# Kernel tuning notes

Hardware: AMD Instinct MI355X
Metric: run time of the kernel (lower is better)

Reference implementation:

```python
import jax, jax.numpy as jnp
import numpy as np
import math

B, T, H, NH, L = 8, 256, 128, 2, 2
DH = H // NH
KC = 3
ITEMNUM = 50000
TIME_SPAN = 256
PERIODS = jnp.array([86400.0, 604800.0, 2592000.0], dtype=jnp.float32)
SCALE_MAGS = [1.0, 1.0, 1.0]
NEG = -1e9


def layernorm(x, g, b, eps=1e-8):
    mu = x.mean(-1, keepdims=True)
    var = ((x - mu) ** 2).mean(-1, keepdims=True)
    return (x - mu) / jnp.sqrt(var + eps) * g + b


def time_encode(t, time_proj):
    # HarmonicTimeEncoding: [sin(2*pi*t/c), cos(2*pi*t/c)] per cycle -> Linear(2K->H, no bias)
    phase = 2.0 * math.pi * t[..., None] / PERIODS
    enc = jnp.concatenate([jnp.sin(phase), jnp.cos(phase)], axis=-1)  # (..., 2K)
    return enc @ time_proj.T


def phase_bias_fn(t, lambdas):
    # PhaseSimilarityBias: per-cycle cosine similarity of (sin,cos) phase vectors
    phase = 2.0 * math.pi * t[..., None] / PERIODS  # (B,T,K)
    phi = jnp.stack([jnp.sin(phase), jnp.cos(phase)], axis=-1)  # (B,T,K,2)
    phi = phi / jnp.maximum(jnp.linalg.norm(phi, axis=-1, keepdims=True), 1e-12)
    sim = jnp.einsum('btkd,bskd->btsk', phi, phi)
    return (sim * lambdas).sum(-1)  # (B,T,T)


def setup_inputs() -> dict:
    key = jax.random.key(0)
    ks = jax.random.split(key, 40)
    def n(i, shape, std=0.02):
        return jax.random.normal(ks[i], shape, dtype=jnp.float32) * std
    inp = {}
    inp['log_seqs'] = jax.random.randint(ks[0], (B, T), 0, ITEMNUM + 1)
    inp['time_matrices'] = jax.random.randint(ks[1], (B, T, T), 0, TIME_SPAN + 1)
    inp['time_seq'] = jnp.sort(jax.random.uniform(ks[2], (B, T), dtype=jnp.float32) * 5e6, axis=-1)
    inp['pos_seqs'] = jax.random.randint(ks[3], (B, T), 1, ITEMNUM + 1)
    inp['neg_seqs'] = jax.random.randint(ks[4], (B, T), 1, ITEMNUM + 1)
    inp['target_times'] = jax.random.uniform(ks[5], (B,), dtype=jnp.float32) * 5e6
    inp['item_emb'] = n(6, (ITEMNUM + 1, H)).at[0].set(0.0)  # padding_idx=0
    inp['abs_pos_K'] = n(7, (T, H))
    inp['abs_pos_V'] = n(8, (T, H))
    inp['time_K_emb'] = n(9, (TIME_SPAN + 1, H))
    inp['time_V_emb'] = n(10, (TIME_SPAN + 1, H))
    inp['Wq'] = n(11, (L, H, H), 0.05); inp['bq'] = jnp.zeros((L, H))
    inp['Wk'] = n(12, (L, H, H), 0.05); inp['bk'] = jnp.zeros((L, H))
    inp['Wv'] = n(13, (L, H, H), 0.05); inp['bv'] = jnp.zeros((L, H))
    inp['attn_ln_g'] = jnp.ones((L, H)); inp['attn_ln_b'] = jnp.zeros((L, H))
    inp['fwd_ln_g'] = jnp.ones((L, H)); inp['fwd_ln_b'] = jnp.zeros((L, H))
    inp['w1'] = n(14, (L, H, H), 0.05); inp['b1'] = jnp.zeros((L, H))
    inp['w2'] = n(15, (L, H, H), 0.05); inp['b2'] = jnp.zeros((L, H))
    inp['last_ln_g'] = jnp.ones((H,)); inp['last_ln_b'] = jnp.zeros((H,))
    inp['time_proj'] = n(16, (H, 2 * KC), 1.0 / math.sqrt(H))
    inp['lambdas'] = jnp.array(SCALE_MAGS, dtype=jnp.float32)
    inp['pred_W'] = n(17, (H, H), 0.05)
    inp['fus_W1'] = n(18, (H, 2 * H), 0.05); inp['fus_b1'] = jnp.zeros((H,))
    inp['fus_W2'] = n(19, (H, H), 0.05); inp['fus_b2'] = jnp.zeros((H,))
    return inp


def reference(log_seqs, time_matrices, time_seq, pos_seqs, neg_seqs, target_times,
              item_emb, abs_pos_K, abs_pos_V, time_K_emb, time_V_emb,
              Wq, bq, Wk, bk, Wv, bv, attn_ln_g, attn_ln_b, fwd_ln_g, fwd_ln_b,
              w1, b1, w2, b2, last_ln_g, last_ln_b, time_proj, lambdas,
              pred_W, fus_W1, fus_b1, fus_W2, fus_b2):
    seqs = item_emb[log_seqs] * math.sqrt(H)
    seqs = seqs + time_encode(time_seq, time_proj)
    tl_mask = (log_seqs == 0)  # (B,T) padding mask
    keep = (~tl_mask)[..., None].astype(seqs.dtype)
    seqs = seqs * keep
    absK = abs_pos_K.reshape(T, NH, DH).transpose(1, 0, 2)  # (NH,T,DH)
    absV = abs_pos_V.reshape(T, NH, DH).transpose(1, 0, 2)
    tK = time_K_emb[time_matrices].reshape(B, T, T, NH, DH)  # (B,T,T,NH,DH)
    tV = time_V_emb[time_matrices].reshape(B, T, T, NH, DH)
    pbias = phase_bias_fn(time_seq, lambdas)  # (B,T,T)
    causal = jnp.triu(jnp.ones((T, T), dtype=bool), k=1)
    mask = causal[None, None] | tl_mask[:, None, None, :]  # (B,1,T,T)
    for l in range(L):
        Qn = layernorm(seqs, attn_ln_g[l], attn_ln_b[l])
        q = (Qn @ Wq[l].T + bq[l]).reshape(B, T, NH, DH).transpose(0, 2, 1, 3)
        k = (seqs @ Wk[l].T + bk[l]).reshape(B, T, NH, DH).transpose(0, 2, 1, 3)
        v = (seqs @ Wv[l].T + bv[l]).reshape(B, T, NH, DH).transpose(0, 2, 1, 3)
        scores = jnp.einsum('bhqd,bhkd->bhqk', q, k)
        scores = scores + jnp.einsum('bhqd,hkd->bhqk', q, absK)
        scores = scores + jnp.einsum('bqkhd,bhqd->bhqk', tK, q)  # relative time-interval term
        scores = scores / math.sqrt(DH) + pbias[:, None]  # phase-similarity logit bias
        scores = jnp.where(mask, NEG, scores)
        A = jax.nn.softmax(scores, axis=-1)
        out = jnp.einsum('bhqk,bhkd->bhqd', A, v)
        out = out + jnp.einsum('bhqk,hkd->bhqd', A, absV)
        out = out + jnp.einsum('bhqk,bqkhd->bhqd', A, tV)
        out = out.transpose(0, 2, 1, 3).reshape(B, T, H)
        seqs = Qn + out
        x = layernorm(seqs, fwd_ln_g[l], fwd_ln_b[l])
        seqs = jax.nn.relu(x @ w1[l].T + b1[l]) @ w2[l].T + b2[l] + x
        seqs = seqs * keep
    log_feats = layernorm(seqs, last_ln_g, last_ln_b)
    H_per = time_encode(target_times, time_proj) @ pred_W.T  # (B,H)
    H_per = jnp.broadcast_to(H_per[:, None], (B, T, H))
    cat = jnp.concatenate([log_feats, H_per], axis=-1)
    fused = jax.nn.gelu(cat @ fus_W1.T + fus_b1, approximate=False) @ fus_W2.T + fus_b2
    pos_logits = (fused * item_emb[pos_seqs]).sum(-1)
    neg_logits = (fused * item_emb[neg_seqs]).sum(-1)
    return (pos_logits, neg_logits)
```

## Files before the change

kernel.cpp:

```cpp
#include <hip/hip_runtime.h>
#include <math.h>

#define TT 256
#define HH 128
#define QT 4

__device__ __forceinline__ void enc6(float t, float e[6]) {
  float x = 6.2831853071795864769f * t;
  float a0 = x / 86400.0f, a1 = x / 604800.0f, a2 = x / 2592000.0f;
  e[0] = sinf(a0); e[1] = sinf(a1); e[2] = sinf(a2);
  e[3] = cosf(a0); e[4] = cosf(a1); e[5] = cosf(a2);
}

__device__ __forceinline__ unsigned short f2bf(float x) {
  unsigned int u = __float_as_uint(x);
  u = (u + 0x7FFFu + ((u >> 16) & 1u)) >> 16;
  return (unsigned short)u;
}

__global__ __launch_bounds__(128) void embed_kernel(
    const int* __restrict__ log_seqs, const float* __restrict__ time_seq,
    const float* __restrict__ item_emb, const float* __restrict__ time_proj,
    float* __restrict__ seqs, float* __restrict__ sc6) {
  int row = blockIdx.x;
  int h = threadIdx.x;
  float t = time_seq[row];
  float e[6]; enc6(t, e);
  int idx = log_seqs[row];
  const float* tp = time_proj + h * 6;
  float val = item_emb[(size_t)idx * HH + h] * 11.313708498984761f;
  val += e[0]*tp[0] + e[1]*tp[1] + e[2]*tp[2] + e[3]*tp[3] + e[4]*tp[4] + e[5]*tp[5];
  seqs[(size_t)row * HH + h] = (idx != 0) ? val : 0.0f;
  if (h < 6) sc6[row * 6 + h] = e[h];
}

__global__ __launch_bounds__(128) void qkv_fused(
    const float* __restrict__ S,
    const float* __restrict__ Wq, const float* __restrict__ bq,
    const float* __restrict__ Wk, const float* __restrict__ bk,
    const float* __restrict__ Wv, const float* __restrict__ bv,
    const float* __restrict__ lng, const float* __restrict__ lnb,
    const float* __restrict__ absK, const float* __restrict__ absV,
    float* __restrict__ QN, float* __restrict__ QB,
    float* __restrict__ KB, float* __restrict__ VB) {
  int which = blockIdx.x >> 8;
  int m0 = (blockIdx.x & 255) * 8;
  int n = threadIdx.x;
  __shared__ float At[8][132];
  __shared__ float mu[8], rs[8];
  #pragma unroll
  for (int r = 0; r < 8; ++r) At[r][n] = S[(size_t)(m0 + r) * HH + n];
  __syncthreads();
  if (which == 0) {
    if (n < 64) {
      int r = n >> 3, sg = n & 7;
      float s = 0.f;
      #pragma unroll
      for (int i = 0; i < 16; ++i) s += At[r][sg * 16 + i];
      s += __shfl_xor(s, 1); s += __shfl_xor(s, 2); s += __shfl_xor(s, 4);
      if (sg == 0) mu[r] = s * (1.0f / HH);
    }
    __syncthreads();
    if (n < 64) {
      int r = n >> 3, sg = n & 7;
      float mm = mu[r], s = 0.f;
      #pragma unroll
      for (int i = 0; i < 16; ++i) { float d = At[r][sg*16+i] - mm; s += d * d; }
      s += __shfl_xor(s, 1); s += __shfl_xor(s, 2); s += __shfl_xor(s, 4);
      if (sg == 0) rs[r] = rsqrtf(s * (1.0f / HH) + 1e-8f);
    }
    __syncthreads();
    float gg = lng[n], bb = lnb[n];
    #pragma unroll
    for (int r = 0; r < 8; ++r) {
      float v = (At[r][n] - mu[r]) * rs[r] * gg + bb;
      At[r][n] = v;
      QN[(size_t)(m0 + r) * HH + n] = v;
    }
    __syncthreads();
  }
  const float* W    = which == 0 ? Wq : which == 1 ? Wk : Wv;
  const float* bias = which == 0 ? bq : which == 1 ? bk : bv;
  const float* addP = which == 1 ? absK : which == 2 ? absV : nullptr;
  float* dst        = which == 0 ? QB : which == 1 ? KB : VB;
  float acc[8];
  #pragma unroll
  for (int r = 0; r < 8; ++r) acc[r] = 0.f;
  const float* wr = W + (size_t)n * HH;
  for (int d = 0; d < HH; d += 4) {
    float4 w = *(const float4*)(wr + d);
    #pragma unroll
    for (int r = 0; r < 8; ++r) {
      float4 a = *(const float4*)(&At[r][d]);
      acc[r] = fmaf(a.x, w.x, fmaf(a.y, w.y, fmaf(a.z, w.z, fmaf(a.w, w.w, acc[r]))));
    }
  }
  float bn = bias[n];
  #pragma unroll
  for (int r = 0; r < 8; ++r) {
    int m = m0 + r;
    float v = acc[r] + bn;
    if (addP) v += addP[(size_t)(m & 255) * HH + n];
    dst[(size_t)m * HH + n] = v;
  }
}

__global__ __launch_bounds__(256) void attn_fused(
    const float* __restrict__ QB, const float* __restrict__ KB,
    const float* __restrict__ VB, const float* __restrict__ QN,
    const int* __restrict__ log_seqs, const int* __restrict__ tmat,
    const float* __restrict__ sc6, const float* __restrict__ tKe,
    const float* __restrict__ tVe, const float* __restrict__ lambdas,
    float* __restrict__ out) {
  int blk = blockIdx.x;
  int qt = blk & 63;
  int h = (blk >> 6) & 1;
  int b = blk >> 7;
  int q0 = qt << 2;
  int hoff = h << 6;
  int tid = threadIdx.x;

  __shared__ unsigned short tKs[257][64];
  __shared__ unsigned short tVs[257][64];
  __shared__ float Qt[QT][64];
  __shared__ float Pp[QT][256];
  __shared__ unsigned short tmq[QT][256];
  __shared__ float sk6[256 * 6];
  __shared__ float sq6[QT * 6];
  __shared__ unsigned char kmask[256];

  for (int idx = tid; idx < 257 * 16; idx += 256) {
    int row = idx >> 4, c4 = (idx & 15) << 2;
    float4 vk = *(const float4*)(tKe + (size_t)row * HH + hoff + c4);
    float4 vv = *(const float4*)(tVe + (size_t)row * HH + hoff + c4);
    uint2 a, c;
    a.x = (unsigned)f2bf(vk.x) | ((unsigned)f2bf(vk.y) << 16);
    a.y = (unsigned)f2bf(vk.z) | ((unsigned)f2bf(vk.w) << 16);
    c.x = (unsigned)f2bf(vv.x) | ((unsigned)f2bf(vv.y) << 16);
    c.y = (unsigned)f2bf(vv.z) | ((unsigned)f2bf(vv.w) << 16);
    *(uint2*)(&tKs[row][c4]) = a;
    *(uint2*)(&tVs[row][c4]) = c;
  }
  for (int idx = tid; idx < 256 * 6; idx += 256)
    sk6[idx] = sc6[(size_t)b * (256 * 6) + idx];
  { int q = tid >> 6, d = tid & 63;
    Qt[q][d] = QB[((size_t)(b * TT + q0 + q)) * HH + hoff + d]; }
  if (tid < QT * 6) sq6[tid] = sc6[((size_t)(b * TT + q0)) * 6 + tid];
  for (int idx = tid; idx < QT * 256; idx += 256) {
    int q = idx >> 8, k = idx & 255;
    tmq[q][k] = (unsigned short)tmat[((size_t)(b * TT + q0 + q)) * TT + k];
  }
  kmask[tid] = (log_seqs[b * TT + tid] == 0) ? 1 : 0;
  __syncthreads();

  int q = tid >> 6;
  int lane = tid & 63;
  int qg = q0 + q;
  float4 qreg[16];
  #pragma unroll
  for (int i = 0; i < 16; ++i) qreg[i] = *(const float4*)(&Qt[q][i << 2]);
  float l0 = lambdas[0], l1 = lambdas[1], l2 = lambdas[2];
  float sA = sq6[q*6+0], sB = sq6[q*6+1], sC = sq6[q*6+2];
  float cA = sq6[q*6+3], cB = sq6[q*6+4], cC = sq6[q*6+5];
  float sarr[4];
  #pragma unroll
  for (int j = 0; j < 4; ++j) {
    int k = lane + (j << 6);
    float sv = -1e9f;
    if (k <= qg && kmask[k] == 0) {
      int tm = tmq[q][k];
      const float* kp = KB + ((size_t)(b * TT + k)) * HH + hoff;
      float acc = 0.f;
      #pragma unroll
      for (int d4 = 0; d4 < 16; ++d4) {
        float4 kv = *(const float4*)(kp + (d4 << 2));
        uint2 tu = *(const uint2*)(&tKs[tm][d4 << 2]);
        float t0 = __uint_as_float(tu.x << 16);
        float t1 = __uint_as_float(tu.x & 0xFFFF0000u);
        float t2 = __uint_as_float(tu.y << 16);
        float t3 = __uint_as_float(tu.y & 0xFFFF0000u);
        float4 qv = qreg[d4];
        acc = fmaf(qv.x, kv.x + t0, acc);
        acc = fmaf(qv.y, kv.y + t1, acc);
        acc = fmaf(qv.z, kv.z + t2, acc);
        acc = fmaf(qv.w, kv.w + t3, acc);
      }
      const float* s6 = &sk6[k * 6];
      float pb = l0 * (sA * s6[0] + cA * s6[3])
               + l1 * (sB * s6[1] + cB * s6[4])
               + l2 * (sC * s6[2] + cC * s6[5]);
      sv = acc * 0.125f + pb;
    }
    sarr[j] = sv;
  }
  float m = fmaxf(fmaxf(sarr[0], sarr[1]), fmaxf(sarr[2], sarr[3]));
  #pragma unroll
  for (int o = 32; o > 0; o >>= 1) m = fmaxf(m, __shfl_xor(m, o));
  float p0 = __expf(sarr[0] - m), p1 = __expf(sarr[1] - m),
        p2 = __expf(sarr[2] - m), p3 = __expf(sarr[3] - m);
  float l = p0 + p1 + p2 + p3;
  #pragma unroll
  for (int o = 32; o > 0; o >>= 1) l += __shfl_xor(l, o);
  float inv = 1.0f / l;
  Pp[q][lane]       = p0 * inv;
  Pp[q][lane + 64]  = p1 * inv;
  Pp[q][lane + 128] = p2 * inv;
  Pp[q][lane + 192] = p3 * inv;
  __syncthreads();

  int kend = (m < -5e8f) ? 256 : (qg + 1);
  float oacc = 0.f;
  const float* vb = VB + ((size_t)(b * TT)) * HH + hoff + lane;
  #pragma unroll 4
  for (int k = 0; k < kend; ++k) {
    float pk = Pp[q][k];
    int tm = tmq[q][k];
    float v = vb[(size_t)k * HH];
    float tv = __uint_as_float(((unsigned)tVs[tm][lane]) << 16);
    oacc = fmaf(pk, v + tv, oacc);
  }
  size_t obase = ((size_t)(b * TT + qg)) * HH + hoff + lane;
  out[obase] = QN[obase] + oacc;
}

__global__ __launch_bounds__(128) void ffn_fused(
    const float* __restrict__ S, const float* __restrict__ W1, const float* __restrict__ b1,
    const float* __restrict__ W2, const float* __restrict__ b2,
    const float* __restrict__ lng, const float* __restrict__ lnb,
    const int* __restrict__ log_seqs, float* __restrict__ outS) {
  int m0 = blockIdx.x * 4;
  int n = threadIdx.x;
  __shared__ float Xt[4][132];
  __shared__ float Ht[4][132];
  __shared__ float mu[4], rs[4];
  #pragma unroll
  for (int r = 0; r < 4; ++r) Xt[r][n] = S[(size_t)(m0 + r) * HH + n];
  __syncthreads();
  if (n < 32) {
    int r = n >> 3, sg = n & 7;
    float s = 0.f;
    #pragma unroll
    for (int i = 0; i < 16; ++i) s += Xt[r][sg * 16 + i];
    s += __shfl_xor(s, 1); s += __shfl_xor(s, 2); s += __shfl_xor(s, 4);
    if (sg == 0) mu[r] = s * (1.0f / HH);
  }
  __syncthreads();
  if (n < 32) {
    int r = n >> 3, sg = n & 7;
    float mm = mu[r], s = 0.f;
    #pragma unroll
    for (int i = 0; i < 16; ++i) { float d = Xt[r][sg*16+i] - mm; s += d * d; }
    s += __shfl_xor(s, 1); s += __shfl_xor(s, 2); s += __shfl_xor(s, 4);
    if (sg == 0) rs[r] = rsqrtf(s * (1.0f / HH) + 1e-8f);
  }
  __syncthreads();
  float gg = lng[n], bb = lnb[n];
  #pragma unroll
  for (int r = 0; r < 4; ++r) Xt[r][n] = (Xt[r][n] - mu[r]) * rs[r] * gg + bb;
  __syncthreads();
  float acc[4] = {0.f, 0.f, 0.f, 0.f};
  const float* wr = W1 + (size_t)n * HH;
  for (int d = 0; d < HH; d += 4) {
    float4 w = *(const float4*)(wr + d);
    #pragma unroll
    for (int r = 0; r < 4; ++r) {
      float4 a = *(const float4*)(&Xt[r][d]);
      acc[r] = fmaf(a.x, w.x, fmaf(a.y, w.y, fmaf(a.z, w.z, fmaf(a.w, w.w, acc[r]))));
    }
  }
  float b1n = b1[n];
  #pragma unroll
  for (int r = 0; r < 4; ++r) Ht[r][n] = fmaxf(acc[r] + b1n, 0.f);
  __syncthreads();
  float acc2[4] = {0.f, 0.f, 0.f, 0.f};
  wr = W2 + (size_t)n * HH;
  for (int d = 0; d < HH; d += 4) {
    float4 w = *(const float4*)(wr + d);
    #pragma unroll
    for (int r = 0; r < 4; ++r) {
      float4 a = *(const float4*)(&Ht[r][d]);
      acc2[r] = fmaf(a.x, w.x, fmaf(a.y, w.y, fmaf(a.z, w.z, fmaf(a.w, w.w, acc2[r]))));
    }
  }
  float b2n = b2[n];
  #pragma unroll
  for (int r = 0; r < 4; ++r) {
    int mrow = m0 + r;
    float v = acc2[r] + b2n + Xt[r][n];
    if (log_seqs[mrow] == 0) v = 0.f;
    outS[(size_t)mrow * HH + n] = v;
  }
}

__global__ __launch_bounds__(128) void hper_kernel(
    const float* __restrict__ target_t, const float* __restrict__ time_proj,
    const float* __restrict__ pred_W, const float* __restrict__ fus_W1,
    const float* __restrict__ fus_b1, float* __restrict__ hp1) {
  int b = blockIdx.x, hth = threadIdx.x;
  __shared__ float te[HH], hp[HH];
  float e[6]; enc6(target_t[b], e);
  const float* tp = time_proj + hth * 6;
  te[hth] = e[0]*tp[0]+e[1]*tp[1]+e[2]*tp[2]+e[3]*tp[3]+e[4]*tp[4]+e[5]*tp[5];
  __syncthreads();
  float u = 0.f;
  const float* pw = pred_W + (size_t)hth * HH;
  for (int d = 0; d < HH; ++d) u += te[d] * pw[d];
  hp[hth] = u;
  __syncthreads();
  float w = fus_b1[hth];
  const float* f1 = fus_W1 + (size_t)hth * 256 + 128;
  for (int d = 0; d < HH; ++d) w += hp[d] * f1[d];
  hp1[b * HH + hth] = w;
}

__global__ __launch_bounds__(128) void final_fused(
    const float* __restrict__ S, const float* __restrict__ lng, const float* __restrict__ lnb,
    const float* __restrict__ fus_W1, const float* __restrict__ HP1,
    const float* __restrict__ fus_W2, const float* __restrict__ fus_b2,
    const float* __restrict__ item_emb, const int* __restrict__ pos,
    const int* __restrict__ neg, float* __restrict__ out) {
  int m0 = blockIdx.x * 4;
  int bidx = m0 >> 8;
  int n = threadIdx.x;
  __shared__ float Xt[4][132];
  __shared__ float Ht[4][132];
  __shared__ float Ft[4][132];
  __shared__ float mu[4], rs[4];
  #pragma unroll
  for (int r = 0; r < 4; ++r) Xt[r][n] = S[(size_t)(m0 + r) * HH + n];
  __syncthreads();
  if (n < 32) {
    int r = n >> 3, sg = n & 7;
    float s = 0.f;
    #pragma unroll
    for (int i = 0; i < 16; ++i) s += Xt[r][sg * 16 + i];
    s += __shfl_xor(s, 1); s += __shfl_xor(s, 2); s += __shfl_xor(s, 4);
    if (sg == 0) mu[r] = s * (1.0f / HH);
  }
  __syncthreads();
  if (n < 32) {
    int r = n >> 3, sg = n & 7;
    float mm = mu[r], s = 0.f;
    #pragma unroll
    for (int i = 0; i < 16; ++i) { float d = Xt[r][sg*16+i] - mm; s += d * d; }
    s += __shfl_xor(s, 1); s += __shfl_xor(s, 2); s += __shfl_xor(s, 4);
    if (sg == 0) rs[r] = rsqrtf(s * (1.0f / HH) + 1e-8f);
  }
  __syncthreads();
  float gg = lng[n], bb = lnb[n];
  #pragma unroll
  for (int r = 0; r < 4; ++r) Xt[r][n] = (Xt[r][n] - mu[r]) * rs[r] * gg + bb;
  __syncthreads();
  float acc[4] = {0.f, 0.f, 0.f, 0.f};
  const float* wr = fus_W1 + (size_t)n * 256;
  for (int d = 0; d < HH; d += 4) {
    float4 w = *(const float4*)(wr + d);
    #pragma unroll
    for (int r = 0; r < 4; ++r) {
      float4 a = *(const float4*)(&Xt[r][d]);
      acc[r] = fmaf(a.x, w.x, fmaf(a.y, w.y, fmaf(a.z, w.z, fmaf(a.w, w.w, acc[r]))));
    }
  }
  float hp = HP1[bidx * HH + n];
  #pragma unroll
  for (int r = 0; r < 4; ++r) {
    float v = acc[r] + hp;
    Ht[r][n] = 0.5f * v * (1.0f + erff(v * 0.70710678118654752f));
  }
  __syncthreads();
  float acc2[4] = {0.f, 0.f, 0.f, 0.f};
  wr = fus_W2 + (size_t)n * HH;
  for (int d = 0; d < HH; d += 4) {
    float4 w = *(const float4*)(wr + d);
    #pragma unroll
    for (int r = 0; r < 4; ++r) {
      float4 a = *(const float4*)(&Ht[r][d]);
      acc2[r] = fmaf(a.x, w.x, fmaf(a.y, w.y, fmaf(a.z, w.z, fmaf(a.w, w.w, acc2[r]))));
    }
  }
  float b2n = fus_b2[n];
  #pragma unroll
  for (int r = 0; r < 4; ++r) Ft[r][n] = acc2[r] + b2n;
  __syncthreads();
  if (n < 64) {
    int task = n >> 3;
    int sg = n & 7;
    int r = task & 3;
    int w = task >> 2;
    int mrow = m0 + r;
    int idx = (w == 0) ? pos[mrow] : neg[mrow];
    const float* ie = item_emb + (size_t)idx * HH;
    float s = 0.f;
    #pragma unroll
    for (int i = 0; i < 16; ++i) s += Ft[r][sg * 16 + i] * ie[sg * 16 + i];
    s += __shfl_xor(s, 1); s += __shfl_xor(s, 2); s += __shfl_xor(s, 4);
    if (sg == 0) out[w * 2048 + mrow] = s;
  }
}

extern "C" void kernel_launch(void* const* d_in, const int* in_sizes, int n_in,
                              void* d_out, int out_size, void* d_ws, size_t ws_size,
                              hipStream_t stream) {
  const int*   log_seqs   = (const int*)d_in[0];
  const int*   tmat       = (const int*)d_in[1];
  const float* time_seq   = (const float*)d_in[2];
  const int*   pos_seqs   = (const int*)d_in[3];
  const int*   neg_seqs   = (const int*)d_in[4];
  const float* target_t   = (const float*)d_in[5];
  const float* item_emb   = (const float*)d_in[6];
  const float* abs_pos_K  = (const float*)d_in[7];
  const float* abs_pos_V  = (const float*)d_in[8];
  const float* time_K_emb = (const float*)d_in[9];
  const float* time_V_emb = (const float*)d_in[10];
  const float* Wq = (const float*)d_in[11];
  const float* bq = (const float*)d_in[12];
  const float* Wk = (const float*)d_in[13];
  const float* bk = (const float*)d_in[14];
  const float* Wv = (const float*)d_in[15];
  const float* bv = (const float*)d_in[16];
  const float* attn_ln_g = (const float*)d_in[17];
  const float* attn_ln_b = (const float*)d_in[18];
  const float* fwd_ln_g = (const float*)d_in[19];
  const float* fwd_ln_b = (const float*)d_in[20];
  const float* w1 = (const float*)d_in[21];
  const float* b1 = (const float*)d_in[22];
  const float* w2 = (const float*)d_in[23];
  const float* b2 = (const float*)d_in[24];
  const float* last_ln_g = (const float*)d_in[25];
  const float* last_ln_b = (const float*)d_in[26];
  const float* time_proj = (const float*)d_in[27];
  const float* lambdas = (const float*)d_in[28];
  const float* pred_W = (const float*)d_in[29];
  const float* fus_W1 = (const float*)d_in[30];
  const float* fus_b1 = (const float*)d_in[31];
  const float* fus_W2 = (const float*)d_in[32];
  const float* fus_b2 = (const float*)d_in[33];
  (void)in_sizes; (void)n_in; (void)out_size; (void)ws_size;

  float* out = (float*)d_out;
  float* ws = (float*)d_ws;
  const int M = 8 * TT;
  float* SC6  = ws;
  float* SEQS = SC6 + M * 6;
  float* QN   = SEQS + M * HH;
  float* QB   = QN + M * HH;
  float* KB   = QB + M * HH;
  float* VB   = KB + M * HH;
  float* HP1  = VB + M * HH;

  embed_kernel<<<M, HH, 0, stream>>>(log_seqs, time_seq, item_emb, time_proj, SEQS, SC6);
  for (int l = 0; l < 2; ++l) {
    const size_t wo = (size_t)l * HH * HH;
    const size_t bo = (size_t)l * HH;
    qkv_fused<<<768, 128, 0, stream>>>(SEQS, Wq + wo, bq + bo, Wk + wo, bk + bo,
                                       Wv + wo, bv + bo, attn_ln_g + bo, attn_ln_b + bo,
                                       abs_pos_K, abs_pos_V, QN, QB, KB, VB);
    attn_fused<<<1024, 256, 0, stream>>>(QB, KB, VB, QN, log_seqs, tmat, SC6,
                                         time_K_emb, time_V_emb, lambdas, SEQS);
    ffn_fused<<<512, 128, 0, stream>>>(SEQS, w1 + wo, b1 + bo, w2 + wo, b2 + bo,
                                       fwd_ln_g + bo, fwd_ln_b + bo, log_seqs, SEQS);
  }
  hper_kernel<<<8, 128, 0, stream>>>(target_t, time_proj, pred_W, fus_W1, fus_b1, HP1);
  final_fused<<<512, 128, 0, stream>>>(SEQS, last_ln_g, last_ln_b, fus_W1, HP1,
                                       fus_W2, fus_b2, item_emb, pos_seqs, neg_seqs, out);
}
```

Measured before the change: 334.2 us.

## Precompute Q·timeK table per query and transpose K for coalesced scores

Adds a pk_gemm kernel that computes, for each query row and head, the dot product of Q with every time-interval key embedding (257 entries), scaled by 1/sqrt(DH). The attention score for a key is then found by indexing this table with the time-matrix value, so the per-block bf16 staging of the time K and V tables into shared memory goes away. K is now stored transposed per (batch, head) so that lanes read consecutive keys with coalesced loads. Time-V values are read straight from global memory in fp32 instead of bf16 LDS. This adds an extra launch and a PK buffer write and read, and the dead first assignment to sv is left in the code.

```diff
diff --git a/kernel.cpp b/kernel.cpp
--- a/kernel.cpp
+++ b/kernel.cpp
@@ -10,12 +10,6 @@
   float a0 = x / 86400.0f, a1 = x / 604800.0f, a2 = x / 2592000.0f;
   e[0] = sinf(a0); e[1] = sinf(a1); e[2] = sinf(a2);
   e[3] = cosf(a0); e[4] = cosf(a1); e[5] = cosf(a2);
-}
-
-__device__ __forceinline__ unsigned short f2bf(float x) {
-  unsigned int u = __float_as_uint(x);
-  u = (u + 0x7FFFu + ((u >> 16) & 1u)) >> 16;
-  return (unsigned short)u;
 }
 
 __global__ __launch_bounds__(128) void embed_kernel(
@@ -42,7 +36,7 @@
     const float* __restrict__ lng, const float* __restrict__ lnb,
     const float* __restrict__ absK, const float* __restrict__ absV,
     float* __restrict__ QN, float* __restrict__ QB,
-    float* __restrict__ KB, float* __restrict__ VB) {
+    float* __restrict__ KT, float* __restrict__ VB) {
   int which = blockIdx.x >> 8;
   int m0 = (blockIdx.x & 255) * 8;
   int n = threadIdx.x;
@@ -82,7 +76,7 @@
   const float* W    = which == 0 ? Wq : which == 1 ? Wk : Wv;
   const float* bias = which == 0 ? bq : which == 1 ? bk : bv;
   const float* addP = which == 1 ? absK : which == 2 ? absV : nullptr;
-  float* dst        = which == 0 ? QB : which == 1 ? KB : VB;
+  float* dst        = which == 0 ? QB : which == 1 ? KT : VB;
   float acc[8];
   #pragma unroll
   for (int r = 0; r < 8; ++r) acc[r] = 0.f;
@@ -101,15 +95,56 @@
     int m = m0 + r;
     float v = acc[r] + bn;
     if (addP) v += addP[(size_t)(m & 255) * HH + n];
-    dst[(size_t)m * HH + n] = v;
+    if (which == 1) {
+      int bb2 = m >> 8, t = m & 255, hh2 = n >> 6, dd = n & 63;
+      dst[(((size_t)(bb2 * 2 + hh2) * 64) + dd) * 256 + t] = v;
+    } else {
+      dst[(size_t)m * HH + n] = v;
+    }
+  }
+}
+
+__global__ __launch_bounds__(256) void pk_gemm(
+    const float* __restrict__ QB, const float* __restrict__ tKe,
+    float* __restrict__ PK) {
+  int blk = blockIdx.x;
+  int qt = blk & 15;
+  int bh = blk >> 4;
+  int h = bh & 1;
+  int b = bh >> 1;
+  int q0 = qt * 16;
+  int hoff = h * 64;
+  int tid = threadIdx.x;
+  __shared__ float Qs[16][64];
+  for (int idx = tid; idx < 16 * 64; idx += 256) {
+    int q = idx >> 6, d = idx & 63;
+    Qs[q][d] = QB[((size_t)(b * TT + q0 + q)) * HH + hoff + d];
+  }
+  __syncthreads();
+  for (int i = tid; i < 257; i += 256) {
+    const float* tp = tKe + (size_t)i * HH + hoff;
+    float acc[16];
+    #pragma unroll
+    for (int q = 0; q < 16; ++q) acc[q] = 0.f;
+    for (int d = 0; d < 64; d += 4) {
+      float4 t4 = *(const float4*)(tp + d);
+      #pragma unroll
+      for (int q = 0; q < 16; ++q) {
+        float4 qv = *(const float4*)(&Qs[q][d]);
+        acc[q] = fmaf(qv.x, t4.x, fmaf(qv.y, t4.y, fmaf(qv.z, t4.z, fmaf(qv.w, t4.w, acc[q]))));
+      }
+    }
+    float* dstp = PK + ((size_t)(bh * TT + q0)) * 257 + i;
+    #pragma unroll
+    for (int q = 0; q < 16; ++q) dstp[(size_t)q * 257] = acc[q] * 0.125f;
   }
 }
 
 __global__ __launch_bounds__(256) void attn_fused(
-    const float* __restrict__ QB, const float* __restrict__ KB,
+    const float* __restrict__ QB, const float* __restrict__ KT,
     const float* __restrict__ VB, const float* __restrict__ QN,
     const int* __restrict__ log_seqs, const int* __restrict__ tmat,
-    const float* __restrict__ sc6, const float* __restrict__ tKe,
+    const float* __restrict__ sc6, const float* __restrict__ PK,
     const float* __restrict__ tVe, const float* __restrict__ lambdas,
     float* __restrict__ out) {
   int blk = blockIdx.x;
@@ -120,32 +155,23 @@
   int hoff = h << 6;
   int tid = threadIdx.x;
 
-  __shared__ unsigned short tKs[257][64];
-  __shared__ unsigned short tVs[257][64];
   __shared__ float Qt[QT][64];
   __shared__ float Pp[QT][256];
+  __shared__ float PKs[QT][260];
   __shared__ unsigned short tmq[QT][256];
   __shared__ float sk6[256 * 6];
   __shared__ float sq6[QT * 6];
   __shared__ unsigned char kmask[256];
 
-  for (int idx = tid; idx < 257 * 16; idx += 256) {
-    int row = idx >> 4, c4 = (idx & 15) << 2;
-    float4 vk = *(const float4*)(tKe + (size_t)row * HH + hoff + c4);
-    float4 vv = *(const float4*)(tVe + (size_t)row * HH + hoff + c4);
-    uint2 a, c;
-    a.x = (unsigned)f2bf(vk.x) | ((unsigned)f2bf(vk.y) << 16);
-    a.y = (unsigned)f2bf(vk.z) | ((unsigned)f2bf(vk.w) << 16);
-    c.x = (unsigned)f2bf(vv.x) | ((unsigned)f2bf(vv.y) << 16);
-    c.y = (unsigned)f2bf(vv.z) | ((unsigned)f2bf(vv.w) << 16);
-    *(uint2*)(&tKs[row][c4]) = a;
-    *(uint2*)(&tVs[row][c4]) = c;
-  }
+  { int q = tid >> 6, d = tid & 63;
+    Qt[q][d] = QB[((size_t)(b * TT + q0 + q)) * HH + hoff + d]; }
   for (int idx = tid; idx < 256 * 6; idx += 256)
     sk6[idx] = sc6[(size_t)b * (256 * 6) + idx];
-  { int q = tid >> 6, d = tid & 63;
-    Qt[q][d] = QB[((size_t)(b * TT + q0 + q)) * HH + hoff + d]; }
   if (tid < QT * 6) sq6[tid] = sc6[((size_t)(b * TT + q0)) * 6 + tid];
+  #pragma unroll
+  for (int q = 0; q < QT; ++q)
+    for (int i = tid; i < 257; i += 256)
+      PKs[q][i] = PK[((size_t)((b * 2 + h) * TT + q0 + q)) * 257 + i];
   for (int idx = tid; idx < QT * 256; idx += 256) {
     int q = idx >> 8, k = idx & 255;
     tmq[q][k] = (unsigned short)tmat[((size_t)(b * TT + q0 + q)) * TT + k];
@@ -162,34 +188,30 @@
   float l0 = lambdas[0], l1 = lambdas[1], l2 = lambdas[2];
   float sA = sq6[q*6+0], sB = sq6[q*6+1], sC = sq6[q*6+2];
   float cA = sq6[q*6+3], cB = sq6[q*6+4], cC = sq6[q*6+5];
+  const float* ktb = KT + ((size_t)((b * 2 + h) * 64)) * 256;
   float sarr[4];
   #pragma unroll
   for (int j = 0; j < 4; ++j) {
     int k = lane + (j << 6);
     float sv = -1e9f;
     if (k <= qg && kmask[k] == 0) {
-      int tm = tmq[q][k];
-      const float* kp = KB + ((size_t)(b * TT + k)) * HH + hoff;
       float acc = 0.f;
       #pragma unroll
       for (int d4 = 0; d4 < 16; ++d4) {
-        float4 kv = *(const float4*)(kp + (d4 << 2));
-        uint2 tu = *(const uint2*)(&tKs[tm][d4 << 2]);
-        float t0 = __uint_as_float(tu.x << 16);
-        float t1 = __uint_as_float(tu.x & 0xFFFF0000u);
-        float t2 = __uint_as_float(tu.y << 16);
-        float t3 = __uint_as_float(tu.y & 0xFFFF0000u);
         float4 qv = qreg[d4];
-        acc = fmaf(qv.x, kv.x + t0, acc);
-        acc = fmaf(qv.y, kv.y + t1, acc);
-        acc = fmaf(qv.z, kv.z + t2, acc);
-        acc = fmaf(qv.w, kv.w + t3, acc);
+        const float* kp = ktb + (size_t)(d4 << 2) * 256 + k;
+        acc = fmaf(qv.x, kp[0],   acc);
+        acc = fmaf(qv.y, kp[256], acc);
+        acc = fmaf(qv.z, kp[512], acc);
+        acc = fmaf(qv.w, kp[768], acc);
       }
+      int tm = tmq[q][k];
       const float* s6 = &sk6[k * 6];
       float pb = l0 * (sA * s6[0] + cA * s6[3])
                + l1 * (sB * s6[1] + cB * s6[4])
                + l2 * (sC * s6[2] + cC * s6[5]);
-      sv = acc * 0.125f + pb;
+      sv = acc + PKs[q][tm] + pb;
+      sv = (acc * 0.125f) + PKs[q][tm] + pb;
     }
     sarr[j] = sv;
   }
@@ -210,14 +232,13 @@
 
   int kend = (m < -5e8f) ? 256 : (qg + 1);
   float oacc = 0.f;
-  const float* vb = VB + ((size_t)(b * TT)) * HH + hoff + lane;
+  const float* vb  = VB + ((size_t)(b * TT)) * HH + hoff + lane;
+  const float* tvb = tVe + hoff + lane;
   #pragma unroll 4
   for (int k = 0; k < kend; ++k) {
     float pk = Pp[q][k];
     int tm = tmq[q][k];
-    float v = vb[(size_t)k * HH];
-    float tv = __uint_as_float(((unsigned)tVs[tm][lane]) << 16);
-    oacc = fmaf(pk, v + tv, oacc);
+    oacc = fmaf(pk, vb[(size_t)k * HH] + tvb[(size_t)tm * HH], oacc);
   }
   size_t obase = ((size_t)(b * TT + qg)) * HH + hoff + lane;
   out[obase] = QN[obase] + oacc;
@@ -444,9 +465,10 @@
   float* SEQS = SC6 + M * 6;
   float* QN   = SEQS + M * HH;
   float* QB   = QN + M * HH;
-  float* KB   = QB + M * HH;
-  float* VB   = KB + M * HH;
+  float* KT   = QB + M * HH;
+  float* VB   = KT + M * HH;
   float* HP1  = VB + M * HH;
+  float* PK   = HP1 + 8 * HH;
 
   embed_kernel<<<M, HH, 0, stream>>>(log_seqs, time_seq, item_emb, time_proj, SEQS, SC6);
   for (int l = 0; l < 2; ++l) {
@@ -454,9 +476,10 @@
     const size_t bo = (size_t)l * HH;
     qkv_fused<<<768, 128, 0, stream>>>(SEQS, Wq + wo, bq + bo, Wk + wo, bk + bo,
                                        Wv + wo, bv + bo, attn_ln_g + bo, attn_ln_b + bo,
-                                       abs_pos_K, abs_pos_V, QN, QB, KB, VB);
-    attn_fused<<<1024, 256, 0, stream>>>(QB, KB, VB, QN, log_seqs, tmat, SC6,
-                                         time_K_emb, time_V_emb, lambdas, SEQS);
+                                       abs_pos_K, abs_pos_V, QN, QB, KT, VB);
+    pk_gemm<<<256, 256, 0, stream>>>(QB, time_K_emb, PK);
+    attn_fused<<<1024, 256, 0, stream>>>(QB, KT, VB, QN, log_seqs, tmat, SC6,
+                                         PK, time_V_emb, lambdas, SEQS);
     ffn_fused<<<512, 128, 0, stream>>>(SEQS, w1 + wo, b1 + bo, w2 + wo, b2 + bo,
                                        fwd_ln_g + bo, fwd_ln_b + bo, log_seqs, SEQS);
   }
```

Measured after the change: 397.5 us. 1.19x slower.
